# Kernel tuning notes

Hardware: AMD Instinct MI355X
Metric: run time of the kernel (lower is better)

## Reference

```python
import jax, jax.numpy as jnp
import numpy as np

N = 50000
E = 800000
IN_DIM = 128
HID = 64
HEADS = 4
OUT_DIM = 64
NEG_SLOPE = 0.2


def setup_inputs() -> dict:
    key = jax.random.key(0)
    ks = jax.random.split(key, 10)
    x = jax.random.normal(ks[0], (N, IN_DIM), dtype=jnp.float32)
    edge_index = jax.random.randint(ks[1], (2, E), 0, N, dtype=jnp.int64)
    s1 = 1.0 / np.sqrt(IN_DIM)
    s2 = 1.0 / np.sqrt(HEADS * HID)
    return {
        "x": x,
        "edge_index": edge_index,
        "W1": jax.random.normal(ks[2], (IN_DIM, HEADS * HID), dtype=jnp.float32) * s1,
        "a_src1": jax.random.normal(ks[3], (HEADS, HID), dtype=jnp.float32) * s2,
        "a_dst1": jax.random.normal(ks[4], (HEADS, HID), dtype=jnp.float32) * s2,
        "b1": jnp.zeros((HEADS * HID,), dtype=jnp.float32),
        "W2": jax.random.normal(ks[5], (HEADS * HID, OUT_DIM), dtype=jnp.float32) * s2,
        "a_src2": jax.random.normal(ks[6], (1, OUT_DIM), dtype=jnp.float32) * 0.125,
        "a_dst2": jax.random.normal(ks[7], (1, OUT_DIM), dtype=jnp.float32) * 0.125,
        "b2": jnp.zeros((OUT_DIM,), dtype=jnp.float32),
    }


def gat_layer(x, src, dst, W, a_src, a_dst, bias, heads, ch, concat):
    n = x.shape[0]
    h = (x @ W).reshape(n, heads, ch)                      # [N,H,C]
    asrc = jnp.einsum('nhc,hc->nh', h, a_src)              # [N,H]
    adst = jnp.einsum('nhc,hc->nh', h, a_dst)              # [N,H]
    e = asrc[src] + adst[dst]                              # [E',H]
    e = jnp.where(e > 0, e, NEG_SLOPE * e)                 # LeakyReLU(0.2)
    # segment softmax over incoming edges of each dst node
    m = jax.ops.segment_max(e, dst, num_segments=n)        # [N,H]
    m = jnp.where(jnp.isfinite(m), m, 0.0)
    ex = jnp.exp(e - m[dst])
    denom = jax.ops.segment_sum(ex, dst, num_segments=n)   # [N,H]
    alpha = ex / (denom[dst] + 1e-16)                      # [E',H]
    out = jax.ops.segment_sum(alpha[:, :, None] * h[src], dst, num_segments=n)  # [N,H,C]
    if concat:
        out = out.reshape(n, heads * ch)
    else:
        out = out.mean(axis=1)
    return out + bias


def reference(x, edge_index, W1, a_src1, a_dst1, b1, W2, a_src2, a_dst2, b2):
    n = x.shape[0]
    loops = jnp.arange(n, dtype=edge_index.dtype)
    src = jnp.concatenate([edge_index[0], loops])          # add self-loops (PyG default)
    dst = jnp.concatenate([edge_index[1], loops])
    h = gat_layer(x, src, dst, W1, a_src1, a_dst1, b1, HEADS, HID, True)
    h = jax.nn.elu(h)
    out = gat_layer(h, src, dst, W2, a_src2, a_dst2, b2, 1, OUT_DIM, False)
    return out
```

## Files before the change

kernel.cpp:

```cpp
#include <hip/hip_runtime.h>
#include <hip/hip_bf16.h>

#define NN 50000
#define EE 800000
#define IN_DIM 128
#define HH 256
#define HID 64
#define HEADS 4
#define OUT_DIM 64
#define SCAN_BLOCKS 196
#define G1_BLOCKS 1563
#define HIST_BLOCKS 3125
#define AGG_BLOCKS 1563
#define TOTW (AGG_BLOCKS * 4)

static __device__ __forceinline__ unsigned short f2bf(float f) {
    unsigned int u = __float_as_uint(f);
    u += 0x7fffu + ((u >> 16) & 1u);
    return (unsigned short)(u >> 16);
}
static __device__ __forceinline__ float bf2f(unsigned short h) {
    return __uint_as_float(((unsigned int)h) << 16);
}


__global__ __launch_bounds__(256) void gemm1_hist_kernel(
    const float* __restrict__ x, const float* __restrict__ W1,
    const float* __restrict__ a_src1, const float* __restrict__ a_dst1,
    unsigned short* __restrict__ h1, float* __restrict__ asrc1, float* __restrict__ adst1,
    const int* __restrict__ ei, int* __restrict__ deg) {
    if (blockIdx.x >= G1_BLOCKS) {
        int e = (blockIdx.x - G1_BLOCKS) * 256 + threadIdx.x;
        atomicAdd(&deg[ei[EE + e]], 1);
        return;
    }
    __shared__ __align__(16) float xs[32][IN_DIM];
    int t = threadIdx.x;
    int row0 = blockIdx.x * 32;
    #pragma unroll
    for (int j = 0; j < 4; j++) {
        int idx = t + j * 256;
        int r = idx >> 5, k4 = (idx & 31) * 4;
        int rr = row0 + r; if (rr >= NN) rr = NN - 1;
        *reinterpret_cast<float4*>(&xs[r][k4]) =
            *reinterpret_cast<const float4*>(&x[(size_t)rr * IN_DIM + k4]);
    }
    __syncthreads();
    int lane = t & 63, wid = t >> 6;
    float4 acc[8];
    #pragma unroll
    for (int r = 0; r < 8; r++) acc[r] = make_float4(0.f, 0.f, 0.f, 0.f);
    const float* wbase = W1 + lane * 4;
    for (int k = 0; k < IN_DIM; k += 4) {
        float4 w0 = *reinterpret_cast<const float4*>(&wbase[(k + 0) * HH]);
        float4 w1 = *reinterpret_cast<const float4*>(&wbase[(k + 1) * HH]);
        float4 w2 = *reinterpret_cast<const float4*>(&wbase[(k + 2) * HH]);
        float4 w3 = *reinterpret_cast<const float4*>(&wbase[(k + 3) * HH]);
        #pragma unroll
        for (int r = 0; r < 8; r++) {
            float4 xv = *reinterpret_cast<const float4*>(&xs[wid * 8 + r][k]);
            acc[r].x = fmaf(xv.x, w0.x, acc[r].x); acc[r].y = fmaf(xv.x, w0.y, acc[r].y);
            acc[r].z = fmaf(xv.x, w0.z, acc[r].z); acc[r].w = fmaf(xv.x, w0.w, acc[r].w);
            acc[r].x = fmaf(xv.y, w1.x, acc[r].x); acc[r].y = fmaf(xv.y, w1.y, acc[r].y);
            acc[r].z = fmaf(xv.y, w1.z, acc[r].z); acc[r].w = fmaf(xv.y, w1.w, acc[r].w);
            acc[r].x = fmaf(xv.z, w2.x, acc[r].x); acc[r].y = fmaf(xv.z, w2.y, acc[r].y);
            acc[r].z = fmaf(xv.z, w2.z, acc[r].z); acc[r].w = fmaf(xv.z, w2.w, acc[r].w);
            acc[r].x = fmaf(xv.w, w3.x, acc[r].x); acc[r].y = fmaf(xv.w, w3.y, acc[r].y);
            acc[r].z = fmaf(xv.w, w3.z, acc[r].z); acc[r].w = fmaf(xv.w, w3.w, acc[r].w);
        }
    }
    float4 asv = *reinterpret_cast<const float4*>(&a_src1[lane * 4]);
    float4 adv = *reinterpret_cast<const float4*>(&a_dst1[lane * 4]);
    int head = lane >> 4;
    #pragma unroll
    for (int r = 0; r < 8; r++) {
        int row = row0 + wid * 8 + r;
        bool ok = row < NN;
        if (ok) {
            ushort4 hv;
            hv.x = f2bf(acc[r].x); hv.y = f2bf(acc[r].y);
            hv.z = f2bf(acc[r].z); hv.w = f2bf(acc[r].w);
            *reinterpret_cast<ushort4*>(&h1[(size_t)row * HH + lane * 4]) = hv;
        }
        float vs = acc[r].x * asv.x + acc[r].y * asv.y + acc[r].z * asv.z + acc[r].w * asv.w;
        float vd = acc[r].x * adv.x + acc[r].y * adv.y + acc[r].z * adv.z + acc[r].w * adv.w;
        #pragma unroll
        for (int o = 1; o < 16; o <<= 1) { vs += __shfl_xor(vs, o); vd += __shfl_xor(vd, o); }
        if (ok && (lane & 15) == 0) {
            asrc1[row * HEADS + head] = vs;
            adst1[row * HEADS + head] = vd;
        }
    }
}


__global__ __launch_bounds__(256) void block_scan_kernel(
    const int* __restrict__ deg, int* __restrict__ local_scan,
    int* __restrict__ block_sum) {
    __shared__ int tmp[256];
    int t = threadIdx.x, i = blockIdx.x * 256 + t;
    int v = (i < NN) ? deg[i] : 0;
    tmp[t] = v;
    __syncthreads();
    for (int d = 1; d < 256; d <<= 1) {
        int u = (t >= d) ? tmp[t - d] : 0;
        __syncthreads();
        tmp[t] += u;
        __syncthreads();
    }
    if (i < NN) local_scan[i] = tmp[t] - v;
    if (t == 255) block_sum[blockIdx.x] = tmp[255];
}

__global__ __launch_bounds__(256) void scan_sums_kernel(int* __restrict__ block_sum) {
    __shared__ int tmp[256];
    int t = threadIdx.x;
    int v = (t < SCAN_BLOCKS) ? block_sum[t] : 0;
    tmp[t] = v;
    __syncthreads();
    for (int d = 1; d < 256; d <<= 1) {
        int u = (t >= d) ? tmp[t - d] : 0;
        __syncthreads();
        tmp[t] += u;
        __syncthreads();
    }
    if (t < SCAN_BLOCKS) block_sum[t] = tmp[t] - v;
}

__global__ __launch_bounds__(256) void finalize_kernel(
    const int* __restrict__ local_scan, const int* __restrict__ block_sum,
    int* __restrict__ row_ptr, int* __restrict__ cursor) {
    int i = blockIdx.x * 256 + threadIdx.x;
    if (i < NN) {
        int v = local_scan[i] + block_sum[blockIdx.x];
        row_ptr[i] = v; cursor[i] = v;
    }
    if (i == 0) row_ptr[NN] = EE;
}

__global__ void scatter_kernel(const int* __restrict__ ei, int* __restrict__ cursor,
                               int* __restrict__ edge_src) {
    int e = blockIdx.x * 256 + threadIdx.x;
    int d = ei[EE + e];
    int pos = atomicAdd(&cursor[d], 1);
    edge_src[pos] = ei[e];
}


__global__ __launch_bounds__(256) void agg1_kernel(
    const int* __restrict__ row_ptr, const int* __restrict__ edge_src,
    const unsigned short* __restrict__ h1, const float* __restrict__ asrc1,
    const float* __restrict__ adst1, const float* __restrict__ b1,
    float* __restrict__ x2) {
    int wid = threadIdx.x >> 6, lane = threadIdx.x & 63;
    int gw = blockIdx.x * 4 + wid;
    int head = lane >> 4;
    unsigned cb = lane * 4;
    const unsigned short* h1l = h1 + cb;
    const float* asl = asrc1 + head;
    float4 bv = *reinterpret_cast<const float4*>(&b1[cb]);
    for (int node = gw; node < NN; node += TOTW) {
        float ad = adst1[node * HEADS + head];
        int beg = row_ptr[node], end = row_ptr[node + 1];
        float denom = 0.f;
        float ax = 0.f, ay = 0.f, az = 0.f, aw = 0.f;
        int s0 = (beg < end) ? edge_src[beg] : node;
        int s1 = (beg + 1 < end) ? edge_src[beg + 1] : node;
        int s2 = (beg + 2 < end) ? edge_src[beg + 2] : node;
        float e0 = asl[(unsigned)s0 * HEADS];
        float e1 = asl[(unsigned)s1 * HEADS];
        float e2 = asl[(unsigned)s2 * HEADS];
        ushort4 h0 = *reinterpret_cast<const ushort4*>(&h1l[(unsigned)s0 * HH]);
        ushort4 h1v = *reinterpret_cast<const ushort4*>(&h1l[(unsigned)s1 * HH]);
        ushort4 h2v = *reinterpret_cast<const ushort4*>(&h1l[(unsigned)s2 * HH]);
        for (int i = beg; i <= end; i++) {
            int j = i + 3;
            int s3 = (j < end) ? edge_src[j] : node;
            float e3 = asl[(unsigned)s3 * HEADS];
            ushort4 h3 = *reinterpret_cast<const ushort4*>(&h1l[(unsigned)s3 * HH]);
            float e = e0 + ad;
            e = fmaxf(e, 0.2f * e);
            float ex = __expf(e);
            denom += ex;
            ax = fmaf(ex, bf2f(h0.x), ax); ay = fmaf(ex, bf2f(h0.y), ay);
            az = fmaf(ex, bf2f(h0.z), az); aw = fmaf(ex, bf2f(h0.w), aw);
            e0 = e1; h0 = h1v;
            e1 = e2; h1v = h2v;
            e2 = e3; h2v = h3;
        }
        float inv = 1.0f / (denom + 1e-16f);
        float v0 = ax * inv + bv.x;
        float v1 = ay * inv + bv.y;
        float v2 = az * inv + bv.z;
        float v3 = aw * inv + bv.w;
        v0 = v0 > 0.f ? v0 : (__expf(v0) - 1.f);
        v1 = v1 > 0.f ? v1 : (__expf(v1) - 1.f);
        v2 = v2 > 0.f ? v2 : (__expf(v2) - 1.f);
        v3 = v3 > 0.f ? v3 : (__expf(v3) - 1.f);
        float4 o; o.x = v0; o.y = v1; o.z = v2; o.w = v3;
        *reinterpret_cast<float4*>(&x2[(size_t)node * HH + cb]) = o;
    }
}


__global__ __launch_bounds__(256) void gemm2_kernel(
    const float* __restrict__ x2, const float* __restrict__ W2,
    const float* __restrict__ a_src2, const float* __restrict__ a_dst2,
    unsigned short* __restrict__ h2, float* __restrict__ asrc2, float* __restrict__ adst2) {
    __shared__ __align__(16) float xs[32][HH];
    int t = threadIdx.x;
    int row0 = blockIdx.x * 32;
    #pragma unroll
    for (int j = 0; j < 8; j++) {
        int idx = t + j * 256;
        int r = idx >> 6, k4 = (idx & 63) * 4;
        int rr = row0 + r; if (rr >= NN) rr = NN - 1;
        *reinterpret_cast<float4*>(&xs[r][k4]) =
            *reinterpret_cast<const float4*>(&x2[(size_t)rr * HH + k4]);
    }
    __syncthreads();
    int c = t & 63, wid = t >> 6;
    float acc[8];
    #pragma unroll
    for (int r = 0; r < 8; r++) acc[r] = 0.f;
    for (int k = 0; k < HH; k += 4) {
        float w0 = W2[(k + 0) * OUT_DIM + c];
        float w1 = W2[(k + 1) * OUT_DIM + c];
        float w2 = W2[(k + 2) * OUT_DIM + c];
        float w3 = W2[(k + 3) * OUT_DIM + c];
        #pragma unroll
        for (int r = 0; r < 8; r++) {
            float4 xv = *reinterpret_cast<const float4*>(&xs[wid * 8 + r][k]);
            acc[r] = fmaf(xv.x, w0, acc[r]);
            acc[r] = fmaf(xv.y, w1, acc[r]);
            acc[r] = fmaf(xv.z, w2, acc[r]);
            acc[r] = fmaf(xv.w, w3, acc[r]);
        }
    }
    float as = a_src2[c], ad = a_dst2[c];
    #pragma unroll
    for (int r = 0; r < 8; r++) {
        int row = row0 + wid * 8 + r;
        bool ok = row < NN;
        if (ok) h2[(size_t)row * OUT_DIM + c] = f2bf(acc[r]);
        float vs = acc[r] * as, vd = acc[r] * ad;
        #pragma unroll
        for (int o = 32; o > 0; o >>= 1) { vs += __shfl_xor(vs, o); vd += __shfl_xor(vd, o); }
        if (ok && c == 0) { asrc2[row] = vs; adst2[row] = vd; }
    }
}


__global__ __launch_bounds__(256) void agg2_kernel(
    const int* __restrict__ row_ptr, const int* __restrict__ edge_src,
    const unsigned short* __restrict__ h2, const float* __restrict__ asrc2,
    const float* __restrict__ adst2, const float* __restrict__ b2,
    float* __restrict__ out) {
    int wid = threadIdx.x >> 6, lane = threadIdx.x & 63;
    int gw = blockIdx.x * 4 + wid;
    const unsigned short* h2l = h2 + lane;
    float bl = b2[lane];
    for (int node = gw; node < NN; node += TOTW) {
        float ad = adst2[node];
        int beg = row_ptr[node], end = row_ptr[node + 1];
        float denom = 0.f, acc = 0.f;
        int s0 = (beg < end) ? edge_src[beg] : node;
        int s1 = (beg + 1 < end) ? edge_src[beg + 1] : node;
        int s2 = (beg + 2 < end) ? edge_src[beg + 2] : node;
        float e0 = asrc2[s0], e1 = asrc2[s1], e2 = asrc2[s2];
        unsigned short h0 = h2l[(unsigned)s0 * OUT_DIM];
        unsigned short h1v = h2l[(unsigned)s1 * OUT_DIM];
        unsigned short h2v = h2l[(unsigned)s2 * OUT_DIM];
        for (int i = beg; i <= end; i++) {
            int j = i + 3;
            int s3 = (j < end) ? edge_src[j] : node;
            float e3 = asrc2[s3];
            unsigned short h3 = h2l[(unsigned)s3 * OUT_DIM];
            float e = e0 + ad;
            e = fmaxf(e, 0.2f * e);
            float ex = __expf(e);
            denom += ex;
            acc = fmaf(ex, bf2f(h0), acc);
            e0 = e1; h0 = h1v;
            e1 = e2; h1v = h2v;
            e2 = e3; h2v = h3;
        }
        out[(size_t)node * OUT_DIM + lane] = acc / (denom + 1e-16f) + bl;
    }
}


extern "C" void kernel_launch(void* const* d_in, const int* in_sizes, int n_in,
                              void* d_out, int out_size, void* d_ws, size_t ws_size,
                              hipStream_t stream) {
    const float* x   = (const float*)d_in[0];
    const int*   ei  = (const int*)d_in[1];
    const float* W1  = (const float*)d_in[2];
    const float* as1 = (const float*)d_in[3];
    const float* ad1 = (const float*)d_in[4];
    const float* b1  = (const float*)d_in[5];
    const float* W2  = (const float*)d_in[6];
    const float* as2 = (const float*)d_in[7];
    const float* ad2 = (const float*)d_in[8];
    const float* b2  = (const float*)d_in[9];
    float* out = (float*)d_out;

    char* ws = (char*)d_ws;
    size_t off = 0;
    auto alloc = [&](size_t bytes) -> void* {
        void* p = ws + off;
        off += (bytes + 255) & ~(size_t)255;
        return p;
    };
    unsigned short* h1 = (unsigned short*)alloc((size_t)NN * HH * 2);
    float* x2     = (float*)alloc((size_t)NN * HH * 4);
    unsigned short* h2 = (unsigned short*)alloc((size_t)NN * OUT_DIM * 2);
    float* asrc1  = (float*)alloc((size_t)NN * HEADS * 4);
    float* adst1  = (float*)alloc((size_t)NN * HEADS * 4);
    float* asrc2  = (float*)alloc((size_t)NN * 4);
    float* adst2  = (float*)alloc((size_t)NN * 4);
    int*   deg    = (int*)alloc((size_t)NN * 4);
    int*   row_ptr= (int*)alloc((size_t)(NN + 1) * 4);
    int*   cursor = (int*)alloc((size_t)NN * 4);
    int*   edge_src=(int*)alloc((size_t)EE * 4);
    int*   local_scan = (int*)alloc((size_t)NN * 4);
    int*   block_sum  = (int*)alloc((size_t)SCAN_BLOCKS * 4);

    hipMemsetAsync(deg, 0, (size_t)NN * 4, stream);
    gemm1_hist_kernel<<<G1_BLOCKS + HIST_BLOCKS, 256, 0, stream>>>(
        x, W1, as1, ad1, h1, asrc1, adst1, ei, deg);
    block_scan_kernel<<<SCAN_BLOCKS, 256, 0, stream>>>(deg, local_scan, block_sum);
    scan_sums_kernel<<<1, 256, 0, stream>>>(block_sum);
    finalize_kernel<<<SCAN_BLOCKS, 256, 0, stream>>>(local_scan, block_sum, row_ptr, cursor);
    scatter_kernel<<<EE / 256, 256, 0, stream>>>(ei, cursor, edge_src);

    agg1_kernel<<<AGG_BLOCKS, 256, 0, stream>>>(row_ptr, edge_src, h1, asrc1, adst1, b1, x2);
    gemm2_kernel<<<(NN + 31) / 32, 256, 0, stream>>>(x2, W2, as2, ad2, h2, asrc2, adst2);
    agg2_kernel<<<AGG_BLOCKS, 256, 0, stream>>>(row_ptr, edge_src, h2, asrc2, adst2, b2, out);
}
```

Measured before the change: 398.3 us.

## Fuse layer-1 aggregation into gemm2 via shared memory, split gemm1 from histogram

Layer-1 aggregation now writes each block's 32 ELU-activated node rows into shared memory, and the layer-2 projection is computed from there in the same kernel. This removes the 51 MB fp32 x2 round-trip through global memory and one kernel launch. Separately, gemm1 is split back out of the degree histogram and retiled to 64 rows per block with 16 accumulators per thread. The fused kernel assigns a fixed 8 nodes per wave with no grid-stride loop, so degree imbalance may leave waves idle. The larger gemm1 tile raises register pressure and doubles its shared memory.

```diff
diff --git a/kernel.cpp b/kernel.cpp
--- a/kernel.cpp
+++ b/kernel.cpp
@@ -9,10 +9,9 @@
 #define HEADS 4
 #define OUT_DIM 64
 #define SCAN_BLOCKS 196
-#define G1_BLOCKS 1563
-#define HIST_BLOCKS 3125
 #define AGG_BLOCKS 1563
 #define TOTW (AGG_BLOCKS * 4)
+#define FUSE_BLOCKS 1563
 
 static __device__ __forceinline__ unsigned short f2bf(float f) {
     unsigned int u = __float_as_uint(f);
@@ -24,75 +23,10 @@
 }
 
 
-__global__ __launch_bounds__(256) void gemm1_hist_kernel(
-    const float* __restrict__ x, const float* __restrict__ W1,
-    const float* __restrict__ a_src1, const float* __restrict__ a_dst1,
-    unsigned short* __restrict__ h1, float* __restrict__ asrc1, float* __restrict__ adst1,
-    const int* __restrict__ ei, int* __restrict__ deg) {
-    if (blockIdx.x >= G1_BLOCKS) {
-        int e = (blockIdx.x - G1_BLOCKS) * 256 + threadIdx.x;
-        atomicAdd(&deg[ei[EE + e]], 1);
-        return;
-    }
-    __shared__ __align__(16) float xs[32][IN_DIM];
-    int t = threadIdx.x;
-    int row0 = blockIdx.x * 32;
-    #pragma unroll
-    for (int j = 0; j < 4; j++) {
-        int idx = t + j * 256;
-        int r = idx >> 5, k4 = (idx & 31) * 4;
-        int rr = row0 + r; if (rr >= NN) rr = NN - 1;
-        *reinterpret_cast<float4*>(&xs[r][k4]) =
-            *reinterpret_cast<const float4*>(&x[(size_t)rr * IN_DIM + k4]);
-    }
-    __syncthreads();
-    int lane = t & 63, wid = t >> 6;
-    float4 acc[8];
-    #pragma unroll
-    for (int r = 0; r < 8; r++) acc[r] = make_float4(0.f, 0.f, 0.f, 0.f);
-    const float* wbase = W1 + lane * 4;
-    for (int k = 0; k < IN_DIM; k += 4) {
-        float4 w0 = *reinterpret_cast<const float4*>(&wbase[(k + 0) * HH]);
-        float4 w1 = *reinterpret_cast<const float4*>(&wbase[(k + 1) * HH]);
-        float4 w2 = *reinterpret_cast<const float4*>(&wbase[(k + 2) * HH]);
-        float4 w3 = *reinterpret_cast<const float4*>(&wbase[(k + 3) * HH]);
-        #pragma unroll
-        for (int r = 0; r < 8; r++) {
-            float4 xv = *reinterpret_cast<const float4*>(&xs[wid * 8 + r][k]);
-            acc[r].x = fmaf(xv.x, w0.x, acc[r].x); acc[r].y = fmaf(xv.x, w0.y, acc[r].y);
-            acc[r].z = fmaf(xv.x, w0.z, acc[r].z); acc[r].w = fmaf(xv.x, w0.w, acc[r].w);
-            acc[r].x = fmaf(xv.y, w1.x, acc[r].x); acc[r].y = fmaf(xv.y, w1.y, acc[r].y);
-            acc[r].z = fmaf(xv.y, w1.z, acc[r].z); acc[r].w = fmaf(xv.y, w1.w, acc[r].w);
-            acc[r].x = fmaf(xv.z, w2.x, acc[r].x); acc[r].y = fmaf(xv.z, w2.y, acc[r].y);
-            acc[r].z = fmaf(xv.z, w2.z, acc[r].z); acc[r].w = fmaf(xv.z, w2.w, acc[r].w);
-            acc[r].x = fmaf(xv.w, w3.x, acc[r].x); acc[r].y = fmaf(xv.w, w3.y, acc[r].y);
-            acc[r].z = fmaf(xv.w, w3.z, acc[r].z); acc[r].w = fmaf(xv.w, w3.w, acc[r].w);
-        }
-    }
-    float4 asv = *reinterpret_cast<const float4*>(&a_src1[lane * 4]);
-    float4 adv = *reinterpret_cast<const float4*>(&a_dst1[lane * 4]);
-    int head = lane >> 4;
-    #pragma unroll
-    for (int r = 0; r < 8; r++) {
-        int row = row0 + wid * 8 + r;
-        bool ok = row < NN;
-        if (ok) {
-            ushort4 hv;
-            hv.x = f2bf(acc[r].x); hv.y = f2bf(acc[r].y);
-            hv.z = f2bf(acc[r].z); hv.w = f2bf(acc[r].w);
-            *reinterpret_cast<ushort4*>(&h1[(size_t)row * HH + lane * 4]) = hv;
-        }
-        float vs = acc[r].x * asv.x + acc[r].y * asv.y + acc[r].z * asv.z + acc[r].w * asv.w;
-        float vd = acc[r].x * adv.x + acc[r].y * adv.y + acc[r].z * adv.z + acc[r].w * adv.w;
-        #pragma unroll
-        for (int o = 1; o < 16; o <<= 1) { vs += __shfl_xor(vs, o); vd += __shfl_xor(vd, o); }
-        if (ok && (lane & 15) == 0) {
-            asrc1[row * HEADS + head] = vs;
-            adst1[row * HEADS + head] = vd;
-        }
-    }
-}
-
+__global__ void hist_kernel(const int* __restrict__ ei, int* __restrict__ deg) {
+    int e = blockIdx.x * 256 + threadIdx.x;
+    atomicAdd(&deg[ei[EE + e]], 1);
+}
 
 __global__ __launch_bounds__(256) void block_scan_kernel(
     const int* __restrict__ deg, int* __restrict__ local_scan,
@@ -147,79 +81,138 @@
 }
 
 
-__global__ __launch_bounds__(256) void agg1_kernel(
+__global__ __launch_bounds__(256) void gemm1_kernel(
+    const float* __restrict__ x, const float* __restrict__ W1,
+    const float* __restrict__ a_src1, const float* __restrict__ a_dst1,
+    unsigned short* __restrict__ h1, float* __restrict__ asrc1, float* __restrict__ adst1) {
+    __shared__ __align__(16) float xs[64][IN_DIM];
+    int t = threadIdx.x;
+    int row0 = blockIdx.x * 64;
+    #pragma unroll
+    for (int j = 0; j < 8; j++) {
+        int idx = t + j * 256;
+        int r = idx >> 5, k4 = (idx & 31) * 4;
+        int rr = row0 + r; if (rr >= NN) rr = NN - 1;
+        *reinterpret_cast<float4*>(&xs[r][k4]) =
+            *reinterpret_cast<const float4*>(&x[(size_t)rr * IN_DIM + k4]);
+    }
+    __syncthreads();
+    int lane = t & 63, wid = t >> 6;
+    float4 acc[16];
+    #pragma unroll
+    for (int r = 0; r < 16; r++) acc[r] = make_float4(0.f, 0.f, 0.f, 0.f);
+    const float* wbase = W1 + lane * 4;
+    for (int k = 0; k < IN_DIM; k += 4) {
+        float4 w0 = *reinterpret_cast<const float4*>(&wbase[(k + 0) * HH]);
+        float4 w1 = *reinterpret_cast<const float4*>(&wbase[(k + 1) * HH]);
+        float4 w2 = *reinterpret_cast<const float4*>(&wbase[(k + 2) * HH]);
+        float4 w3 = *reinterpret_cast<const float4*>(&wbase[(k + 3) * HH]);
+        #pragma unroll
+        for (int r = 0; r < 16; r++) {
+            float4 xv = *reinterpret_cast<const float4*>(&xs[wid * 16 + r][k]);
+            acc[r].x = fmaf(xv.x, w0.x, acc[r].x); acc[r].y = fmaf(xv.x, w0.y, acc[r].y);
+            acc[r].z = fmaf(xv.x, w0.z, acc[r].z); acc[r].w = fmaf(xv.x, w0.w, acc[r].w);
+            acc[r].x = fmaf(xv.y, w1.x, acc[r].x); acc[r].y = fmaf(xv.y, w1.y, acc[r].y);
+            acc[r].z = fmaf(xv.y, w1.z, acc[r].z); acc[r].w = fmaf(xv.y, w1.w, acc[r].w);
+            acc[r].x = fmaf(xv.z, w2.x, acc[r].x); acc[r].y = fmaf(xv.z, w2.y, acc[r].y);
+            acc[r].z = fmaf(xv.z, w2.z, acc[r].z); acc[r].w = fmaf(xv.z, w2.w, acc[r].w);
+            acc[r].x = fmaf(xv.w, w3.x, acc[r].x); acc[r].y = fmaf(xv.w, w3.y, acc[r].y);
+            acc[r].z = fmaf(xv.w, w3.z, acc[r].z); acc[r].w = fmaf(xv.w, w3.w, acc[r].w);
+        }
+    }
+    float4 asv = *reinterpret_cast<const float4*>(&a_src1[lane * 4]);
+    float4 adv = *reinterpret_cast<const float4*>(&a_dst1[lane * 4]);
+    int head = lane >> 4;
+    #pragma unroll
+    for (int r = 0; r < 16; r++) {
+        int row = row0 + wid * 16 + r;
+        bool ok = row < NN;
+        if (ok) {
+            ushort4 hv;
+            hv.x = f2bf(acc[r].x); hv.y = f2bf(acc[r].y);
+            hv.z = f2bf(acc[r].z); hv.w = f2bf(acc[r].w);
+            *reinterpret_cast<ushort4*>(&h1[(size_t)row * HH + lane * 4]) = hv;
+        }
+        float vs = acc[r].x * asv.x + acc[r].y * asv.y + acc[r].z * asv.z + acc[r].w * asv.w;
+        float vd = acc[r].x * adv.x + acc[r].y * adv.y + acc[r].z * adv.z + acc[r].w * adv.w;
+        #pragma unroll
+        for (int o = 1; o < 16; o <<= 1) { vs += __shfl_xor(vs, o); vd += __shfl_xor(vd, o); }
+        if (ok && (lane & 15) == 0) {
+            asrc1[row * HEADS + head] = vs;
+            adst1[row * HEADS + head] = vd;
+        }
+    }
+}
+
+
+__global__ __launch_bounds__(256) void agg1_gemm2_kernel(
     const int* __restrict__ row_ptr, const int* __restrict__ edge_src,
     const unsigned short* __restrict__ h1, const float* __restrict__ asrc1,
     const float* __restrict__ adst1, const float* __restrict__ b1,
-    float* __restrict__ x2) {
-    int wid = threadIdx.x >> 6, lane = threadIdx.x & 63;
-    int gw = blockIdx.x * 4 + wid;
+    const float* __restrict__ W2, const float* __restrict__ a_src2,
+    const float* __restrict__ a_dst2,
+    unsigned short* __restrict__ h2, float* __restrict__ asrc2, float* __restrict__ adst2) {
+    __shared__ __align__(16) float xs[32][HH];
+    int t = threadIdx.x;
+    int lane = t & 63, wid = t >> 6;
+    int row0 = blockIdx.x * 32;
     int head = lane >> 4;
     unsigned cb = lane * 4;
     const unsigned short* h1l = h1 + cb;
     const float* asl = asrc1 + head;
     float4 bv = *reinterpret_cast<const float4*>(&b1[cb]);
-    for (int node = gw; node < NN; node += TOTW) {
-        float ad = adst1[node * HEADS + head];
-        int beg = row_ptr[node], end = row_ptr[node + 1];
-        float denom = 0.f;
-        float ax = 0.f, ay = 0.f, az = 0.f, aw = 0.f;
-        int s0 = (beg < end) ? edge_src[beg] : node;
-        int s1 = (beg + 1 < end) ? edge_src[beg + 1] : node;
-        int s2 = (beg + 2 < end) ? edge_src[beg + 2] : node;
-        float e0 = asl[(unsigned)s0 * HEADS];
-        float e1 = asl[(unsigned)s1 * HEADS];
-        float e2 = asl[(unsigned)s2 * HEADS];
-        ushort4 h0 = *reinterpret_cast<const ushort4*>(&h1l[(unsigned)s0 * HH]);
-        ushort4 h1v = *reinterpret_cast<const ushort4*>(&h1l[(unsigned)s1 * HH]);
-        ushort4 h2v = *reinterpret_cast<const ushort4*>(&h1l[(unsigned)s2 * HH]);
-        for (int i = beg; i <= end; i++) {
-            int j = i + 3;
-            int s3 = (j < end) ? edge_src[j] : node;
-            float e3 = asl[(unsigned)s3 * HEADS];
-            ushort4 h3 = *reinterpret_cast<const ushort4*>(&h1l[(unsigned)s3 * HH]);
-            float e = e0 + ad;
-            e = fmaxf(e, 0.2f * e);
-            float ex = __expf(e);
-            denom += ex;
-            ax = fmaf(ex, bf2f(h0.x), ax); ay = fmaf(ex, bf2f(h0.y), ay);
-            az = fmaf(ex, bf2f(h0.z), az); aw = fmaf(ex, bf2f(h0.w), aw);
-            e0 = e1; h0 = h1v;
-            e1 = e2; h1v = h2v;
-            e2 = e3; h2v = h3;
-        }
-        float inv = 1.0f / (denom + 1e-16f);
-        float v0 = ax * inv + bv.x;
-        float v1 = ay * inv + bv.y;
-        float v2 = az * inv + bv.z;
-        float v3 = aw * inv + bv.w;
-        v0 = v0 > 0.f ? v0 : (__expf(v0) - 1.f);
-        v1 = v1 > 0.f ? v1 : (__expf(v1) - 1.f);
-        v2 = v2 > 0.f ? v2 : (__expf(v2) - 1.f);
-        v3 = v3 > 0.f ? v3 : (__expf(v3) - 1.f);
-        float4 o; o.x = v0; o.y = v1; o.z = v2; o.w = v3;
-        *reinterpret_cast<float4*>(&x2[(size_t)node * HH + cb]) = o;
-    }
-}
-
-
-__global__ __launch_bounds__(256) void gemm2_kernel(
-    const float* __restrict__ x2, const float* __restrict__ W2,
-    const float* __restrict__ a_src2, const float* __restrict__ a_dst2,
-    unsigned short* __restrict__ h2, float* __restrict__ asrc2, float* __restrict__ adst2) {
-    __shared__ __align__(16) float xs[32][HH];
-    int t = threadIdx.x;
-    int row0 = blockIdx.x * 32;
-    #pragma unroll
-    for (int j = 0; j < 8; j++) {
-        int idx = t + j * 256;
-        int r = idx >> 6, k4 = (idx & 63) * 4;
-        int rr = row0 + r; if (rr >= NN) rr = NN - 1;
-        *reinterpret_cast<float4*>(&xs[r][k4]) =
-            *reinterpret_cast<const float4*>(&x2[(size_t)rr * HH + k4]);
+
+    #pragma unroll 1
+    for (int r = 0; r < 8; r++) {
+        int node = row0 + wid * 8 + r;
+        if (node < NN) {
+            float ad = adst1[node * HEADS + head];
+            int beg = row_ptr[node], end = row_ptr[node + 1];
+            float denom = 0.f;
+            float ax = 0.f, ay = 0.f, az = 0.f, aw = 0.f;
+            int s0 = (beg < end) ? edge_src[beg] : node;
+            int s1 = (beg + 1 < end) ? edge_src[beg + 1] : node;
+            int s2 = (beg + 2 < end) ? edge_src[beg + 2] : node;
+            float e0 = asl[(unsigned)s0 * HEADS];
+            float e1 = asl[(unsigned)s1 * HEADS];
+            float e2 = asl[(unsigned)s2 * HEADS];
+            ushort4 h0 = *reinterpret_cast<const ushort4*>(&h1l[(unsigned)s0 * HH]);
+            ushort4 h1v = *reinterpret_cast<const ushort4*>(&h1l[(unsigned)s1 * HH]);
+            ushort4 h2v = *reinterpret_cast<const ushort4*>(&h1l[(unsigned)s2 * HH]);
+            for (int i = beg; i <= end; i++) {
+                int j = i + 3;
+                int s3 = (j < end) ? edge_src[j] : node;
+                float e3 = asl[(unsigned)s3 * HEADS];
+                ushort4 h3 = *reinterpret_cast<const ushort4*>(&h1l[(unsigned)s3 * HH]);
+                float e = e0 + ad;
+                e = fmaxf(e, 0.2f * e);
+                float ex = __expf(e);
+                denom += ex;
+                ax = fmaf(ex, bf2f(h0.x), ax); ay = fmaf(ex, bf2f(h0.y), ay);
+                az = fmaf(ex, bf2f(h0.z), az); aw = fmaf(ex, bf2f(h0.w), aw);
+                e0 = e1; h0 = h1v;
+                e1 = e2; h1v = h2v;
+                e2 = e3; h2v = h3;
+            }
+            float inv = 1.0f / (denom + 1e-16f);
+            float v0 = ax * inv + bv.x;
+            float v1 = ay * inv + bv.y;
+            float v2 = az * inv + bv.z;
+            float v3 = aw * inv + bv.w;
+            v0 = v0 > 0.f ? v0 : (__expf(v0) - 1.f);
+            v1 = v1 > 0.f ? v1 : (__expf(v1) - 1.f);
+            v2 = v2 > 0.f ? v2 : (__expf(v2) - 1.f);
+            v3 = v3 > 0.f ? v3 : (__expf(v3) - 1.f);
+            float4 o; o.x = v0; o.y = v1; o.z = v2; o.w = v3;
+            *reinterpret_cast<float4*>(&xs[wid * 8 + r][cb]) = o;
+        } else {
+            float4 z = make_float4(0.f, 0.f, 0.f, 0.f);
+            *reinterpret_cast<float4*>(&xs[wid * 8 + r][cb]) = z;
+        }
     }
     __syncthreads();
-    int c = t & 63, wid = t >> 6;
+
+    int c = lane;
     float acc[8];
     #pragma unroll
     for (int r = 0; r < 8; r++) acc[r] = 0.f;
@@ -237,13 +230,13 @@
             acc[r] = fmaf(xv.w, w3, acc[r]);
         }
     }
-    float as = a_src2[c], ad = a_dst2[c];
+    float as = a_src2[c], ad2v = a_dst2[c];
     #pragma unroll
     for (int r = 0; r < 8; r++) {
         int row = row0 + wid * 8 + r;
         bool ok = row < NN;
         if (ok) h2[(size_t)row * OUT_DIM + c] = f2bf(acc[r]);
-        float vs = acc[r] * as, vd = acc[r] * ad;
+        float vs = acc[r] * as, vd = acc[r] * ad2v;
         #pragma unroll
         for (int o = 32; o > 0; o >>= 1) { vs += __shfl_xor(vs, o); vd += __shfl_xor(vd, o); }
         if (ok && c == 0) { asrc2[row] = vs; adst2[row] = vd; }
@@ -313,7 +306,6 @@
         return p;
     };
     unsigned short* h1 = (unsigned short*)alloc((size_t)NN * HH * 2);
-    float* x2     = (float*)alloc((size_t)NN * HH * 4);
     unsigned short* h2 = (unsigned short*)alloc((size_t)NN * OUT_DIM * 2);
     float* asrc1  = (float*)alloc((size_t)NN * HEADS * 4);
     float* adst1  = (float*)alloc((size_t)NN * HEADS * 4);
@@ -327,14 +319,14 @@
     int*   block_sum  = (int*)alloc((size_t)SCAN_BLOCKS * 4);
 
     hipMemsetAsync(deg, 0, (size_t)NN * 4, stream);
-    gemm1_hist_kernel<<<G1_BLOCKS + HIST_BLOCKS, 256, 0, stream>>>(
-        x, W1, as1, ad1, h1, asrc1, adst1, ei, deg);
+    hist_kernel<<<EE / 256, 256, 0, stream>>>(ei, deg);
     block_scan_kernel<<<SCAN_BLOCKS, 256, 0, stream>>>(deg, local_scan, block_sum);
     scan_sums_kernel<<<1, 256, 0, stream>>>(block_sum);
     finalize_kernel<<<SCAN_BLOCKS, 256, 0, stream>>>(local_scan, block_sum, row_ptr, cursor);
     scatter_kernel<<<EE / 256, 256, 0, stream>>>(ei, cursor, edge_src);
 
-    agg1_kernel<<<AGG_BLOCKS, 256, 0, stream>>>(row_ptr, edge_src, h1, asrc1, adst1, b1, x2);
-    gemm2_kernel<<<(NN + 31) / 32, 256, 0, stream>>>(x2, W2, as2, ad2, h2, asrc2, adst2);
+    gemm1_kernel<<<(NN + 63) / 64, 256, 0, stream>>>(x, W1, as1, ad1, h1, asrc1, adst1);
+    agg1_gemm2_kernel<<<FUSE_BLOCKS, 256, 0, stream>>>(
+        row_ptr, edge_src, h1, asrc1, adst1, b1, W2, as2, ad2, h2, asrc2, adst2);
     agg2_kernel<<<AGG_BLOCKS, 256, 0, stream>>>(row_ptr, edge_src, h2, asrc2, adst2, b2, out);
 }
```

After: 447.4 us. 1.12x slower.
